# Optimization experiments

Hardware: AMD Instinct MI355X
Metric: run time of the kernel (lower is better)

Reference implementation:

```python
import jax, jax.numpy as jnp
import numpy as np

B, S, H = 8, 2048, 1024


def setup_inputs() -> dict:
    key = jax.random.key(0)
    ks = jax.random.split(key, 12)
    s = 1.0 / np.sqrt(H)
    return {
        "_q": jax.random.normal(ks[0], (B, S, H), jnp.float32),
        "_kv": jax.random.normal(ks[1], (B, S, H), jnp.float32),
        "W_kv": jax.random.normal(ks[2], (H, 2 * H), jnp.float32) * s,
        "b_kv": jnp.zeros((2 * H,), jnp.float32),
        "W_q": jax.random.normal(ks[3], (H, H), jnp.float32) * s,
        "b_q": jnp.zeros((H,), jnp.float32),
        "W1": jax.random.normal(ks[4], (H, 4 * H), jnp.float32) * s,
        "b1": jnp.zeros((4 * H,), jnp.float32),
        "W2": jax.random.normal(ks[5], (4 * H, H), jnp.float32) * (1.0 / np.sqrt(4 * H)),
        "b2": jnp.zeros((H,), jnp.float32),
    }


def reference(_q, _kv, W_kv, b_kv, W_q, b_q, W1, b1, W2, b2):
    # kv projection then split into k, v: [B,S,H] each
    kv = _kv @ W_kv + b_kv
    k, v = jnp.split(kv, 2, axis=-1)
    q = _q @ W_q + b_q
    # NOTE: original module does single-head attention with NO 1/sqrt(d) scale
    scores = jnp.einsum('bqh,bkh->bqk', q, k)          # [B,Sq,Sk]
    attn = jax.nn.softmax(scores, axis=-1)
    out = jnp.einsum('bqk,bkh->bqh', attn, v)          # [B,Sq,H]
    # MLP: Linear -> exact GELU -> (Dropout=identity in eval) -> Linear
    hidden = jax.nn.gelu(out @ W1 + b1, approximate=False)
    return hidden @ W2 + b2
```

## Files before the change

### kernel.cpp

```cpp
#include <hip/hip_runtime.h>
#include <hip/hip_bf16.h>

typedef __attribute__((ext_vector_type(8))) short short8;
typedef __attribute__((ext_vector_type(8))) _Float16 half8;
typedef __attribute__((ext_vector_type(4))) _Float16 half4v;
typedef __attribute__((ext_vector_type(4))) float f32x4;
typedef unsigned short us;

#define GLDS16(G, L) __builtin_amdgcn_global_load_lds( \
    (const __attribute__((address_space(1))) void*)(G), \
    (__attribute__((address_space(3))) void*)(L), 16, 0, 0)

__global__ void k_sentinel(float* p) {
    if (threadIdx.x == 0 && blockIdx.x == 0) p[0] = 12345.0f;
}

__device__ __forceinline__ float fast_gelu(float x) {
    float ax = fabsf(x) * 0.70710678118654752f;
    float t = __frcp_rn(fmaf(0.3275911f, ax, 1.0f));
    float p = fmaf(1.061405429f, t, -1.453152027f);
    p = fmaf(p, t, 1.421413741f);
    p = fmaf(p, t, -0.284496736f);
    p = fmaf(p, t, 0.254829592f);
    p = p * t * __expf(-ax * ax);
    float erfv = __builtin_copysignf(1.0f - p, x);
    return 0.5f * x * (1.0f + erfv);
}

__global__ void k_cast(const float* __restrict__ in, _Float16* __restrict__ out, long n4) {
    long i = (long)blockIdx.x * blockDim.x + threadIdx.x;
    long stride = (long)gridDim.x * blockDim.x;
    for (; i < n4; i += stride) {
        float4 v = ((const float4*)in)[i];
        half4v h;
        h[0] = (_Float16)v.x; h[1] = (_Float16)v.y;
        h[2] = (_Float16)v.z; h[3] = (_Float16)v.w;
        ((half4v*)out)[i] = h;
    }
}

__global__ void k_wtransh(const float* __restrict__ in, _Float16* __restrict__ out,
                          int K, int N) {
    __shared__ float tile[32][33];
    int n0 = blockIdx.x * 32, k0 = blockIdx.y * 32;
    int tx = threadIdx.x, ty = threadIdx.y;
#pragma unroll
    for (int r = ty; r < 32; r += 8)
        tile[r][tx] = in[(size_t)(k0 + r) * N + n0 + tx];
    __syncthreads();
#pragma unroll
    for (int r = ty; r < 32; r += 8)
        out[(size_t)(n0 + r) * K + k0 + tx] = (_Float16)tile[tx][r];
}

__device__ __forceinline__ float wredmax(float v) {
#pragma unroll
    for (int off = 32; off > 0; off >>= 1) v = fmaxf(v, __shfl_xor(v, off, 64));
    return v;
}
__device__ __forceinline__ float wredsum(float v) {
#pragma unroll
    for (int off = 32; off > 0; off >>= 1) v += __shfl_xor(v, off, 64);
    return v;
}

__global__ __launch_bounds__(256) void k_softmax(const float* __restrict__ S,
                                                 _Float16* __restrict__ P) {
    __shared__ float red[8];
    size_t base = (size_t)blockIdx.x * 2048;
    int t = threadIdx.x;
    float4 a = ((const float4*)(S + base))[2 * t];
    float4 b = ((const float4*)(S + base))[2 * t + 1];
    float v[8] = {a.x, a.y, a.z, a.w, b.x, b.y, b.z, b.w};
    float m = v[0];
#pragma unroll
    for (int j = 1; j < 8; j++) m = fmaxf(m, v[j]);
    m = wredmax(m);
    int wv = t >> 6;
    if ((t & 63) == 0) red[wv] = m;
    __syncthreads();
    m = fmaxf(fmaxf(red[0], red[1]), fmaxf(red[2], red[3]));
    float s = 0.f;
#pragma unroll
    for (int j = 0; j < 8; j++) { v[j] = __expf(v[j] - m); s += v[j]; }
    s = wredsum(s);
    if ((t & 63) == 0) red[4 + wv] = s;
    __syncthreads();
    s = red[4] + red[5] + red[6] + red[7];
    float inv = 1.f / s;
    half4v o0, o1;
#pragma unroll
    for (int j = 0; j < 4; j++) o0[j] = (_Float16)(v[j] * inv);
#pragma unroll
    for (int j = 0; j < 4; j++) o1[j] = (_Float16)(v[4 + j] * inv);
    ((half4v*)(P + base))[2 * t] = o0;
    ((half4v*)(P + base))[2 * t + 1] = o1;
}

template <int OUT_MODE, bool GELU_ACT>
__global__ __launch_bounds__(256, 2) void k_gemm64(
    const us* __restrict__ A, const us* __restrict__ B,
    const float* __restrict__ bias, void* __restrict__ C,
    int N, int K, long sA, long sB, long sC) {
    __shared__ __align__(16) us ldsA[8192];
    __shared__ __align__(16) us ldsB[8192];

    const int tid = threadIdx.x;
    const int wave = tid >> 6, lane = tid & 63;
    const int wr = wave >> 1, wc = wave & 1;
    const int l15 = lane & 15, l4 = lane >> 4;
    const int m0 = blockIdx.x * 128, n0 = blockIdx.y * 128;

    const us* pA = A + (size_t)blockIdx.z * sA;
    const us* pB = B + (size_t)blockIdx.z * sB;
    const size_t zC = (size_t)blockIdx.z * sC;

    f32x4 acc[4][4] = {};

    auto stage = [&](const us* __restrict__ g, us* l, int r0, int kk) {
#pragma unroll
        for (int i = 0; i < 4; i++) {
            int s = (i << 8) + tid;
            int row = s >> 3;
            int cl = (s & 7) ^ (row & 7);
            const us* src = g + (size_t)(r0 + row) * K + kk + (cl << 3);
            us* dst = l + (((i << 8) + (wave << 6)) << 3);
            GLDS16(src, dst);
        }
    };

    for (int kk = 0; kk < K; kk += 64) {
        stage(pA, ldsA, m0, kk);
        stage(pB, ldsB, n0, kk);
        __syncthreads();

#pragma unroll
        for (int ks = 0; ks < 2; ks++) {
            short8 af[4], bf[4];
#pragma unroll
            for (int f = 0; f < 4; f++) {
                int ra = (wr << 6) + (f << 4) + l15;
                af[f] = *(const short8*)(
                    &ldsA[(ra << 6) + ((((ks << 2) | l4) ^ (ra & 7)) << 3)]);
                int rb = (wc << 6) + (f << 4) + l15;
                bf[f] = *(const short8*)(
                    &ldsB[(rb << 6) + ((((ks << 2) | l4) ^ (rb & 7)) << 3)]);
            }
#pragma unroll
            for (int fm = 0; fm < 4; fm++)
#pragma unroll
                for (int fn = 0; fn < 4; fn++)
                    acc[fm][fn] = __builtin_amdgcn_mfma_f32_16x16x32_f16(
                        __builtin_bit_cast(half8, af[fm]), __builtin_bit_cast(half8, bf[fn]),
                        acc[fm][fn], 0, 0, 0);
        }
        __syncthreads();
    }

    float bv[4];
#pragma unroll
    for (int fn = 0; fn < 4; fn++)
        bv[fn] = bias ? bias[n0 + (wc << 6) + (fn << 4) + l15] : 0.f;

#pragma unroll
    for (int fm = 0; fm < 4; fm++) {
        int rbase = m0 + (wr << 6) + (fm << 4) + (l4 << 2);
#pragma unroll
        for (int fn = 0; fn < 4; fn++) {
            int col = n0 + (wc << 6) + (fn << 4) + l15;
#pragma unroll
            for (int r = 0; r < 4; r++) {
                float x = acc[fm][fn][r] + bv[fn];
                if (GELU_ACT) x = fast_gelu(x);
                size_t row = (size_t)(rbase + r);
                if (OUT_MODE == 5) {
                    size_t o = ((row >> 11) * (size_t)N + (size_t)col) * 2048 + (row & 2047);
                    ((_Float16*)C)[o] = (_Float16)x;
                } else {
                    size_t o = zC + row * N + col;
                    if (OUT_MODE == 0) ((float*)C)[o] = x;
                    else               ((_Float16*)C)[o] = (_Float16)x;
                }
            }
        }
    }
}

template <int OUT_MODE, bool GELU_ACT>
__global__ __launch_bounds__(256, 2) void k_gemmdb(
    const us* __restrict__ A, const us* __restrict__ B,
    const float* __restrict__ bias, void* __restrict__ C,
    int N, int K, long sA, long sB, long sC) {
    __shared__ __align__(16) us lds[2][2][8192];

    const int tid = threadIdx.x;
    const int wave = tid >> 6, lane = tid & 63;
    const int wr = wave >> 1, wc = wave & 1;
    const int l15 = lane & 15, l4 = lane >> 4;
    const int m0 = blockIdx.x * 128, n0 = blockIdx.y * 128;

    const us* pA = A + (size_t)blockIdx.z * sA;
    const us* pB = B + (size_t)blockIdx.z * sB;
    const size_t zC = (size_t)blockIdx.z * sC;

    f32x4 acc[4][4] = {};

    auto stage = [&](const us* __restrict__ g, us* l, int r0, int kk) {
#pragma unroll
        for (int i = 0; i < 4; i++) {
            int s = (i << 8) + tid;
            int row = s >> 3;
            int cl = (s & 7) ^ (row & 7);
            const us* src = g + (size_t)(r0 + row) * K + kk + (cl << 3);
            us* dst = l + (((i << 8) + (wave << 6)) << 3);
            GLDS16(src, dst);
        }
    };

    stage(pA, &lds[0][0][0], m0, 0);
    stage(pB, &lds[0][1][0], n0, 0);

    const int NT = K >> 6;
    for (int t = 0; t < NT; ++t) {
        const int cur = t & 1;
        if (t + 1 < NT) {
            stage(pA, &lds[cur ^ 1][0][0], m0, (t + 1) << 6);
            stage(pB, &lds[cur ^ 1][1][0], n0, (t + 1) << 6);
            __builtin_amdgcn_sched_barrier(0);
            asm volatile("s_waitcnt vmcnt(8)" ::: "memory");
        } else {
            asm volatile("s_waitcnt vmcnt(0)" ::: "memory");
        }
        __builtin_amdgcn_s_barrier();
        __builtin_amdgcn_sched_barrier(0);

        const us* la = &lds[cur][0][0];
        const us* lb = &lds[cur][1][0];
#pragma unroll
        for (int ks = 0; ks < 2; ks++) {
            short8 af[4], bf[4];
#pragma unroll
            for (int f = 0; f < 4; f++) {
                int ra = (wr << 6) + (f << 4) + l15;
                af[f] = *(const short8*)(&la[(ra << 6) + ((((ks << 2) | l4) ^ (ra & 7)) << 3)]);
                int rb = (wc << 6) + (f << 4) + l15;
                bf[f] = *(const short8*)(&lb[(rb << 6) + ((((ks << 2) | l4) ^ (rb & 7)) << 3)]);
            }
            __builtin_amdgcn_s_setprio(1);
#pragma unroll
            for (int fm = 0; fm < 4; fm++)
#pragma unroll
                for (int fn = 0; fn < 4; fn++)
                    acc[fm][fn] = __builtin_amdgcn_mfma_f32_16x16x32_f16(
                        __builtin_bit_cast(half8, af[fm]), __builtin_bit_cast(half8, bf[fn]),
                        acc[fm][fn], 0, 0, 0);
            __builtin_amdgcn_s_setprio(0);
        }
        __builtin_amdgcn_sched_barrier(0);
        __builtin_amdgcn_s_barrier();
    }

    float bv[4];
#pragma unroll
    for (int fn = 0; fn < 4; fn++)
        bv[fn] = bias ? bias[n0 + (wc << 6) + (fn << 4) + l15] : 0.f;

#pragma unroll
    for (int fm = 0; fm < 4; fm++) {
        int rbase = m0 + (wr << 6) + (fm << 4) + (l4 << 2);
#pragma unroll
        for (int fn = 0; fn < 4; fn++) {
            int col = n0 + (wc << 6) + (fn << 4) + l15;
#pragma unroll
            for (int r = 0; r < 4; r++) {
                float x = acc[fm][fn][r] + bv[fn];
                if (GELU_ACT) x = fast_gelu(x);
                size_t row = (size_t)(rbase + r);
                size_t o = zC + row * N + col;
                if (OUT_MODE == 0) ((float*)C)[o] = x;
                else               ((_Float16*)C)[o] = (_Float16)x;
            }
        }
    }
}

extern "C" void kernel_launch(void* const* d_in, const int* in_sizes, int n_in,
                              void* d_out, int out_size, void* d_ws, size_t ws_size,
                              hipStream_t stream) {
    (void)in_sizes; (void)n_in; (void)out_size;
    const float* g_q   = (const float*)d_in[0];
    const float* g_kv  = (const float*)d_in[1];
    const float* g_Wkv = (const float*)d_in[2];
    const float* g_bkv = (const float*)d_in[3];
    const float* g_Wq  = (const float*)d_in[4];
    const float* g_bq  = (const float*)d_in[5];
    const float* g_W1  = (const float*)d_in[6];
    const float* g_b1  = (const float*)d_in[7];
    const float* g_W2  = (const float*)d_in[8];
    const float* g_b2  = (const float*)d_in[9];

    const size_t MiB = 1048576ull;
    const long SH = 2048L * 1024;
    const long SS = 2048L * 2048;
    char* ws = (char*)d_ws;
    dim3 tb32(32, 8);

    if (ws_size < 176 * MiB) {
        k_sentinel<<<1, 64, 0, stream>>>((float*)d_out);
        return;
    }

    _Float16* xq  = (_Float16*)ws;
    char*     REGION = ws + 32 * MiB;
    _Float16* kf    = (_Float16*)REGION;
    _Float16* vT    = (_Float16*)(REGION + 32 * MiB);
    _Float16* P_all = (_Float16*)(REGION + 64 * MiB);
    _Float16* hidden = (_Float16*)REGION;
    char* wreg = ws + 160 * MiB;
    _Float16* WkvT = (_Float16*)wreg;
    _Float16* WqT  = (_Float16*)(wreg + 4 * MiB);
    _Float16* W1T  = (_Float16*)wreg;
    _Float16* W2T  = (_Float16*)(wreg + 8 * MiB);

    _Float16* xkv      = (_Float16*)d_out;
    float*    scores_c = (float*)d_out;
    _Float16* q_all    = (_Float16*)((char*)d_out + 32 * MiB);

    k_wtransh<<<dim3(64, 32), tb32, 0, stream>>>(g_Wkv, WkvT, 1024, 2048);
    k_wtransh<<<dim3(32, 32), tb32, 0, stream>>>(g_Wq, WqT, 1024, 1024);
    k_cast<<<4096, 256, 0, stream>>>(g_kv, xkv, 4194304);
    k_cast<<<4096, 256, 0, stream>>>(g_q, xq, 4194304);

    k_gemm64<4, false><<<dim3(128, 8, 1), 256, 0, stream>>>(
        (const us*)xkv, (const us*)WkvT, g_bkv, kf, 1024, 1024, 0, 0, 0);
    k_gemm64<5, false><<<dim3(128, 8, 1), 256, 0, stream>>>(
        (const us*)xkv, (const us*)(WkvT + (size_t)1024 * 1024), g_bkv + 1024, vT,
        1024, 1024, 0, 0, 0);
    k_gemm64<4, false><<<dim3(128, 8, 1), 256, 0, stream>>>(
        (const us*)xq, (const us*)WqT, g_bq, q_all, 1024, 1024, 0, 0, 0);

    for (int c = 0; c < 4; ++c) {
        size_t ro = (size_t)c * 4096 * 1024;
        k_gemm64<0, false><<<dim3(16, 16, 2), 256, 0, stream>>>(
            (const us*)(q_all + ro), (const us*)(kf + ro), nullptr, scores_c,
            2048, 1024, SH, SH, SS);
        k_softmax<<<4096, 256, 0, stream>>>(scores_c, P_all + (size_t)c * 2 * SS);
    }

    k_gemm64<4, false><<<dim3(16, 8, 8), 256, 0, stream>>>(
        (const us*)P_all, (const us*)vT, nullptr, xq, 1024, 2048, SS, SH, SH);

    k_wtransh<<<dim3(128, 32), tb32, 0, stream>>>(g_W1, W1T, 1024, 4096);
    k_wtransh<<<dim3(32, 128), tb32, 0, stream>>>(g_W2, W2T, 4096, 1024);
    k_gemmdb<4, true><<<dim3(128, 32, 1), 256, 0, stream>>>(
        (const us*)xq, (const us*)W1T, g_b1, hidden, 4096, 1024, 0, 0, 0);
    k_gemmdb<0, false><<<dim3(128, 8, 1), 256, 0, stream>>>(
        (const us*)hidden, (const us*)W2T, g_b2, d_out, 1024, 4096, 0, 0, 0);
}
```

Baseline: 733.9 us.

## Switch MLP GEMMs to 32x32x16 MFMA with single-buffered LDS

```diff
diff --git a/kernel.cpp b/kernel.cpp
--- a/kernel.cpp
+++ b/kernel.cpp
@@ -5,6 +5,7 @@
 typedef __attribute__((ext_vector_type(8))) _Float16 half8;
 typedef __attribute__((ext_vector_type(4))) _Float16 half4v;
 typedef __attribute__((ext_vector_type(4))) float f32x4;
+typedef __attribute__((ext_vector_type(16))) float f32x16;
 typedef unsigned short us;
 
 #define GLDS16(G, L) __builtin_amdgcn_global_load_lds( \
@@ -187,23 +188,24 @@
 }
 
 template <int OUT_MODE, bool GELU_ACT>
-__global__ __launch_bounds__(256, 2) void k_gemmdb(
+__global__ __launch_bounds__(256, 2) void k_gemm32(
     const us* __restrict__ A, const us* __restrict__ B,
     const float* __restrict__ bias, void* __restrict__ C,
     int N, int K, long sA, long sB, long sC) {
-    __shared__ __align__(16) us lds[2][2][8192];
+    __shared__ __align__(16) us ldsA[8192];
+    __shared__ __align__(16) us ldsB[8192];
 
     const int tid = threadIdx.x;
     const int wave = tid >> 6, lane = tid & 63;
     const int wr = wave >> 1, wc = wave & 1;
-    const int l15 = lane & 15, l4 = lane >> 4;
+    const int l31 = lane & 31, l5 = lane >> 5;
     const int m0 = blockIdx.x * 128, n0 = blockIdx.y * 128;
 
     const us* pA = A + (size_t)blockIdx.z * sA;
     const us* pB = B + (size_t)blockIdx.z * sB;
     const size_t zC = (size_t)blockIdx.z * sC;
 
-    f32x4 acc[4][4] = {};
+    f32x16 acc[2][2] = {};
 
     auto stage = [&](const us* __restrict__ g, us* l, int r0, int kk) {
 #pragma unroll
@@ -217,65 +219,50 @@
         }
     };
 
-    stage(pA, &lds[0][0][0], m0, 0);
-    stage(pB, &lds[0][1][0], n0, 0);
-
-    const int NT = K >> 6;
-    for (int t = 0; t < NT; ++t) {
-        const int cur = t & 1;
-        if (t + 1 < NT) {
-            stage(pA, &lds[cur ^ 1][0][0], m0, (t + 1) << 6);
-            stage(pB, &lds[cur ^ 1][1][0], n0, (t + 1) << 6);
-            __builtin_amdgcn_sched_barrier(0);
-            asm volatile("s_waitcnt vmcnt(8)" ::: "memory");
-        } else {
-            asm volatile("s_waitcnt vmcnt(0)" ::: "memory");
-        }
-        __builtin_amdgcn_s_barrier();
-        __builtin_amdgcn_sched_barrier(0);
-
-        const us* la = &lds[cur][0][0];
-        const us* lb = &lds[cur][1][0];
-#pragma unroll
-        for (int ks = 0; ks < 2; ks++) {
-            short8 af[4], bf[4];
-#pragma unroll
-            for (int f = 0; f < 4; f++) {
-                int ra = (wr << 6) + (f << 4) + l15;
-                af[f] = *(const short8*)(&la[(ra << 6) + ((((ks << 2) | l4) ^ (ra & 7)) << 3)]);
-                int rb = (wc << 6) + (f << 4) + l15;
-                bf[f] = *(const short8*)(&lb[(rb << 6) + ((((ks << 2) | l4) ^ (rb & 7)) << 3)]);
+    for (int kk = 0; kk < K; kk += 64) {
+        stage(pA, ldsA, m0, kk);
+        stage(pB, ldsB, n0, kk);
+        __syncthreads();
+
+#pragma unroll
+        for (int ks = 0; ks < 4; ks++) {
+            short8 af[2], bf[2];
+#pragma unroll
+            for (int f = 0; f < 2; f++) {
+                int ra = (wr << 6) + (f << 5) + l31;
+                af[f] = *(const short8*)(
+                    &ldsA[(ra << 6) + ((((ks << 1) | l5) ^ (ra & 7)) << 3)]);
+                int rb = (wc << 6) + (f << 5) + l31;
+                bf[f] = *(const short8*)(
+                    &ldsB[(rb << 6) + ((((ks << 1) | l5) ^ (rb & 7)) << 3)]);
             }
-            __builtin_amdgcn_s_setprio(1);
-#pragma unroll
-            for (int fm = 0; fm < 4; fm++)
-#pragma unroll
-                for (int fn = 0; fn < 4; fn++)
-                    acc[fm][fn] = __builtin_amdgcn_mfma_f32_16x16x32_f16(
+#pragma unroll
+            for (int fm = 0; fm < 2; fm++)
+#pragma unroll
+                for (int fn = 0; fn < 2; fn++)
+                    acc[fm][fn] = __builtin_amdgcn_mfma_f32_32x32x16_f16(
                         __builtin_bit_cast(half8, af[fm]), __builtin_bit_cast(half8, bf[fn]),
                         acc[fm][fn], 0, 0, 0);
-            __builtin_amdgcn_s_setprio(0);
-        }
-        __builtin_amdgcn_sched_barrier(0);
-        __builtin_amdgcn_s_barrier();
-    }
-
-    float bv[4];
-#pragma unroll
-    for (int fn = 0; fn < 4; fn++)
-        bv[fn] = bias ? bias[n0 + (wc << 6) + (fn << 4) + l15] : 0.f;
-
-#pragma unroll
-    for (int fm = 0; fm < 4; fm++) {
-        int rbase = m0 + (wr << 6) + (fm << 4) + (l4 << 2);
-#pragma unroll
-        for (int fn = 0; fn < 4; fn++) {
-            int col = n0 + (wc << 6) + (fn << 4) + l15;
-#pragma unroll
-            for (int r = 0; r < 4; r++) {
+        }
+        __syncthreads();
+    }
+
+    float bv[2];
+#pragma unroll
+    for (int fn = 0; fn < 2; fn++)
+        bv[fn] = bias ? bias[n0 + (wc << 6) + (fn << 5) + l31] : 0.f;
+
+#pragma unroll
+    for (int fm = 0; fm < 2; fm++) {
+        int rbase = m0 + (wr << 6) + (fm << 5) + (l5 << 2);
+#pragma unroll
+        for (int fn = 0; fn < 2; fn++) {
+            int col = n0 + (wc << 6) + (fn << 5) + l31;
+#pragma unroll
+            for (int r = 0; r < 16; r++) {
                 float x = acc[fm][fn][r] + bv[fn];
                 if (GELU_ACT) x = fast_gelu(x);
-                size_t row = (size_t)(rbase + r);
+                size_t row = (size_t)(rbase + (r & 3) + ((r >> 2) << 3));
                 size_t o = zC + row * N + col;
                 if (OUT_MODE == 0) ((float*)C)[o] = x;
                 else               ((_Float16*)C)[o] = (_Float16)x;
@@ -352,8 +339,8 @@
 
     k_wtransh<<<dim3(128, 32), tb32, 0, stream>>>(g_W1, W1T, 1024, 4096);
     k_wtransh<<<dim3(32, 128), tb32, 0, stream>>>(g_W2, W2T, 4096, 1024);
-    k_gemmdb<4, true><<<dim3(128, 32, 1), 256, 0, stream>>>(
+    k_gemm32<4, true><<<dim3(128, 32, 1), 256, 0, stream>>>(
         (const us*)xq, (const us*)W1T, g_b1, hidden, 4096, 1024, 0, 0, 0);
-    k_gemmdb<0, false><<<dim3(128, 8, 1), 256, 0, stream>>>(
+    k_gemm32<0, false><<<dim3(128, 8, 1), 256, 0, stream>>>(
         (const us*)hidden, (const us*)W2T, g_b2, d_out, 1024, 4096, 0, 0, 0);
 }
```

Measured after the change: 759.5 us. 3.5% more time.
